# Performance work log

Measured on AMD Instinct MI355X. Metric: run time of the kernel, lower is better.

The kernel has to match this reference:

```python
import jax, jax.numpy as jnp
import numpy as np

N_NODES = 50000
N_EDGES = 800000
N_GRAPHS = 64
IN_DIM = 128
HID4 = 256  # hidden_dim * 4
OUT_DIM = 256
EPS = 1e-5


def setup_inputs() -> dict:
    key = jax.random.key(0)
    ks = jax.random.split(key, 11)
    x = jax.random.normal(ks[0], (N_NODES, IN_DIM), jnp.float32)
    w = jax.random.uniform(ks[1], (N_EDGES,), jnp.float32)
    src = jax.random.randint(ks[2], (N_EDGES,), 0, N_NODES, dtype=jnp.int32)
    dst = jax.random.randint(ks[3], (N_EDGES,), 0, N_NODES, dtype=jnp.int32)
    graph_ids = jnp.sort(jax.random.randint(ks[4], (N_NODES,), 0, N_GRAPHS, dtype=jnp.int32))
    W1 = jax.random.normal(ks[5], (IN_DIM, HID4), jnp.float32) * 0.05
    Wfc = jax.random.normal(ks[6], (IN_DIM, HID4), jnp.float32) * 0.05
    gamma = jnp.ones((HID4,), jnp.float32)
    beta = jnp.zeros((HID4,), jnp.float32)
    W2 = jax.random.normal(ks[7], (2 * HID4, HID4), jnp.float32) * 0.05
    W3 = jax.random.normal(ks[8], (HID4, OUT_DIM), jnp.float32) * 0.05
    return {"x": x, "w": w, "W1": W1, "Wfc": Wfc, "gamma": gamma, "beta": beta,
            "W2": W2, "W3": W3, "src": src, "dst": dst, "graph_ids": graph_ids}


def _agg(h, src, dst, w, n):
    # edge-weighted SpMM: sum_{e: dst(e)=v} w_e * h[src(e)]
    return jax.ops.segment_sum(h[src] * w[:, None], dst, num_segments=n)


def _graph_conv(h, W, src, dst, w, out_norm, in_norm, n):
    # DGL GraphConv, norm='both', no bias, with edge_weight.
    h = h * out_norm  # D_out^{-1/2} on source side
    din, dout = W.shape
    if din > dout:  # DGL applies W first when it shrinks the width
        h = _agg(h @ W, src, dst, w, n)
    else:
        h = _agg(h, src, dst, w, n) @ W
    return h * in_norm  # D_in^{-1/2} on destination side


def _layer_norm(h, gamma, beta):
    mu = jnp.mean(h, axis=-1, keepdims=True)
    var = jnp.var(h, axis=-1, keepdims=True)
    return (h - mu) * jax.lax.rsqrt(var + EPS) * gamma + beta


def reference(x, w, W1, Wfc, gamma, beta, W2, W3, src, dst, graph_ids):
    n = x.shape[0]
    ones_e = jnp.ones(src.shape[0], jnp.float32)
    out_deg = jnp.maximum(jax.ops.segment_sum(ones_e, src, num_segments=n), 1.0)
    in_deg = jnp.maximum(jax.ops.segment_sum(ones_e, dst, num_segments=n), 1.0)
    out_norm = (out_deg ** -0.5)[:, None]
    in_norm = (in_deg ** -0.5)[:, None]

    x1 = jax.nn.relu(_graph_conv(x, W1, src, dst, w, out_norm, in_norm, n))
    f1 = jax.nn.relu(_layer_norm(x @ Wfc, gamma, beta))
    x1f1 = jnp.concatenate((x1, f1), axis=1)  # [N, 512]
    x2 = jax.nn.relu(_graph_conv(x1f1, W2, src, dst, w, out_norm, in_norm, n))
    x3 = jax.nn.relu(_graph_conv(x2, W3, src, dst, w, out_norm, in_norm, n))
    # dgl.sum_nodes: per-graph segment-sum readout
    readout = jax.ops.segment_sum(x3, graph_ids, num_segments=N_GRAPHS)
    return readout
```

## Files before the change

kernel.cpp:

```cpp
#include <hip/hip_runtime.h>

#define NN 50000
#define NE 800000
#define NG 64
#define EPSF 1e-5f

typedef __bf16 bf16x8 __attribute__((ext_vector_type(8)));
typedef float f32x4 __attribute__((ext_vector_type(4)));

#define AS1 __attribute__((address_space(1)))
#define AS3 __attribute__((address_space(3)))

__device__ __forceinline__ void gl_lds16(const unsigned short* g, unsigned short* l) {
#if __has_builtin(__builtin_amdgcn_global_load_lds)
  __builtin_amdgcn_global_load_lds((const AS1 void*)g, (AS3 void*)l, 16, 0, 0);
#else
  *(uint4*)l = *(const uint4*)g;
#endif
}

__device__ __forceinline__ unsigned short f2bf(float f) {
  unsigned u = __builtin_bit_cast(unsigned, f);
  u += 0x7fff + ((u >> 16) & 1);
  return (unsigned short)(u >> 16);
}
__device__ __forceinline__ float bf_lo(unsigned u) {
  return __builtin_bit_cast(float, u << 16);
}
__device__ __forceinline__ float bf_hi(unsigned u) {
  return __builtin_bit_cast(float, u & 0xffff0000u);
}

#define NB_H 64
#define EC   12500
#define HWORDS 12500
#define XB   1563
#define XTOT 1600000
#define WTB  256
__global__ __launch_bounds__(1024) void prep_kernel(
    const int* __restrict__ src, const int* __restrict__ dst,
    unsigned char* __restrict__ hout, unsigned char* __restrict__ hin,
    int* __restrict__ rank,
    const float* __restrict__ x, unsigned short* __restrict__ xb,
    const float* __restrict__ W1, const float* __restrict__ Wfc,
    const float* __restrict__ W2, const float* __restrict__ W3,
    unsigned short* __restrict__ W1t, unsigned short* __restrict__ Wfct,
    unsigned short* __restrict__ W2t, unsigned short* __restrict__ W3t) {
  __shared__ unsigned hist[HWORDS];
  int b = blockIdx.x;
  int tid = threadIdx.x;
  if (b < NB_H) {
    int e0 = b * EC;
#pragma unroll
    for (int ph = 0; ph < 2; ph++) {
      const int* key = ph ? src : dst;
      unsigned char* gh = (ph ? hout : hin) + (size_t)b * NN;
      for (int i = tid; i < HWORDS; i += 1024) hist[i] = 0u;
      __syncthreads();
      for (int i = tid; i < EC; i += 1024) {
        int k = key[e0 + i];
        int sh = (k & 3) << 3;
        unsigned old = atomicAdd(&hist[k >> 2], 1u << sh);
        if (ph == 0) rank[e0 + i] = (int)((old >> sh) & 0xffu);
      }
      __syncthreads();
      unsigned* gw = (unsigned*)gh;
      for (int i = tid; i < HWORDS; i += 1024) gw[i] = hist[i];
      __syncthreads();
    }
  } else if (b < NB_H + XB) {
    int i = (b - NB_H) * 1024 + tid;
    if (i < XTOT) {
      float4 v = ((const float4*)x)[i];
      uint2 pk;
      pk.x = (unsigned)f2bf(v.x) | ((unsigned)f2bf(v.y) << 16);
      pk.y = (unsigned)f2bf(v.z) | ((unsigned)f2bf(v.w) << 16);
      ((uint2*)xb)[i] = pk;
    }
  } else {
    int i = (b - NB_H - XB) * 1024 + tid;
    const float* W; unsigned short* Wt; int K, local;
    if (i < 32768)       { W = W1;  Wt = W1t;  K = 128; local = i; }
    else if (i < 65536)  { W = Wfc; Wt = Wfct; K = 128; local = i - 32768; }
    else if (i < 196608) { W = W2;  Wt = W2t;  K = 512; local = i - 65536; }
    else                 { W = W3;  Wt = W3t;  K = 256; local = i - 196608; }
    int n = local / K, k = local - n * K;
    Wt[local] = f2bf(W[(size_t)k * 256 + n]);
  }
}

__global__ void norms_scan1(const unsigned char* __restrict__ hout,
                            unsigned char* __restrict__ hin,
                            int* __restrict__ din,
                            float* __restrict__ onorm, float* __restrict__ inorm,
                            int* __restrict__ bsum, int n) {
  int i = blockIdx.x * 256 + threadIdx.x;
  int d = 0;
  if (i < n) {
    int a = 0;
    for (int b = 0; b < NB_H; b++) a += hout[(size_t)b * NN + i];
    int run = 0;
    for (int b = 0; b < NB_H; b++) {
      int t = hin[(size_t)b * NN + i];
      hin[(size_t)b * NN + i] = (unsigned char)run;
      run += t;
    }
    d = run;
    din[i] = run;
    onorm[i] = rsqrtf((float)(a > 1 ? a : 1));
    inorm[i] = rsqrtf((float)(d > 1 ? d : 1));
  }
  int v = d;
#pragma unroll
  for (int off = 32; off > 0; off >>= 1) v += __shfl_down(v, off);
  __shared__ int ws[4];
  int wave = threadIdx.x >> 6, lane = threadIdx.x & 63;
  if (lane == 0) ws[wave] = v;
  __syncthreads();
  if (threadIdx.x == 0) bsum[blockIdx.x] = ws[0] + ws[1] + ws[2] + ws[3];
}

__global__ void scan3_kernel(const int* __restrict__ din, const int* __restrict__ bsum,
                             int* __restrict__ rp, int n, int nb) {
  int t = threadIdx.x;
  int lane = t & 63, wave = t >> 6;
  int bj = (t < nb) ? bsum[t] : 0;
  int pre = (t < (int)blockIdx.x) ? bj : 0;
  int p = pre, q = bj;
#pragma unroll
  for (int off = 32; off > 0; off >>= 1) {
    p += __shfl_down(p, off);
    q += __shfl_down(q, off);
  }
  __shared__ int red[8];
  __shared__ int baseS, totS;
  if (lane == 0) { red[wave] = p; red[4 + wave] = q; }
  __syncthreads();
  if (t == 0) {
    baseS = red[0] + red[1] + red[2] + red[3];
    totS  = red[4] + red[5] + red[6] + red[7];
  }
  __syncthreads();
  int i = blockIdx.x * 256 + t;
  int v = (i < n) ? din[i] : 0;
  __shared__ int tmp[256];
  tmp[t] = v;
  __syncthreads();
  for (int off = 1; off < 256; off <<= 1) {
    int x = (t >= off) ? tmp[t - off] : 0;
    __syncthreads();
    tmp[t] += x;
    __syncthreads();
  }
  if (i < n) rp[i] = tmp[t] - v + baseS;
  if (blockIdx.x == gridDim.x - 1 && t == 0) rp[n] = totS;
}

__global__ void fill_kernel(const int* __restrict__ src, const int* __restrict__ dst,
                            const float* __restrict__ w, const float* __restrict__ onorm,
                            const float* __restrict__ inorm,
                            const int* __restrict__ rp, const int* __restrict__ rank,
                            const unsigned char* __restrict__ binBase,
                            uint2* __restrict__ edge, int E) {
  int e = blockIdx.x * 256 + threadIdx.x;
  if (e < E) {
    int d = dst[e], s = src[e];
    int b = e / EC;
    int pos = rp[d] + (int)binBase[(size_t)b * NN + d] + rank[e];
    float wv = w[e] * onorm[s] * inorm[d];
    edge[pos] = make_uint2((unsigned)s, __builtin_bit_cast(unsigned, wv));
  }
}

template <int RELU, int NU>
__global__ __launch_bounds__(64) void spmm_bf16(
    const unsigned short* __restrict__ feat, int ldf,
    const int* __restrict__ rp, const uint2* __restrict__ edge,
    unsigned short* __restrict__ out, int ldo) {
  int v = blockIdx.x;
  int t = threadIdx.x;
  int beg = rp[v], end = rp[v + 1];
  float acc[2 * NU];
#pragma unroll
  for (int i = 0; i < 2 * NU; i++) acc[i] = 0.f;
  const unsigned short* base = feat + t * (2 * NU);
  int e = beg;
  for (; e + 8 <= end; e += 8) {
    int s[8]; float ww[8];
#pragma unroll
    for (int k = 0; k < 8; k++) {
      uint2 q = edge[e + k];
      s[k] = (int)q.x;
      ww[k] = __builtin_bit_cast(float, q.y);
    }
    unsigned u[8][NU];
#pragma unroll
    for (int k = 0; k < 8; k++) {
      const unsigned* pr = (const unsigned*)&base[(size_t)s[k] * ldf];
      if (NU == 2) { uint2 q = *(const uint2*)pr; u[k][0] = q.x; u[k][NU - 1] = q.y; }
      else u[k][0] = pr[0];
    }
#pragma unroll
    for (int k = 0; k < 8; k++)
#pragma unroll
      for (int j = 0; j < NU; j++) {
        acc[2 * j]     += ww[k] * bf_lo(u[k][j]);
        acc[2 * j + 1] += ww[k] * bf_hi(u[k][j]);
      }
  }
  for (; e < end; e++) {
    uint2 qe = edge[e];
    float w0 = __builtin_bit_cast(float, qe.y);
    const unsigned* pr = (const unsigned*)&base[(size_t)qe.x * ldf];
    unsigned u[NU];
    if (NU == 2) { uint2 q = *(const uint2*)pr; u[0] = q.x; u[NU - 1] = q.y; }
    else u[0] = pr[0];
#pragma unroll
    for (int j = 0; j < NU; j++) {
      acc[2 * j]     += w0 * bf_lo(u[j]);
      acc[2 * j + 1] += w0 * bf_hi(u[j]);
    }
  }
  unsigned o[NU];
#pragma unroll
  for (int j = 0; j < NU; j++) {
    float a = acc[2 * j], b = acc[2 * j + 1];
    if (RELU) { a = fmaxf(a, 0.f); b = fmaxf(b, 0.f); }
    o[j] = (unsigned)f2bf(a) | ((unsigned)f2bf(b) << 16);
  }
  unsigned* po = (unsigned*)&out[(size_t)v * ldo + t * (2 * NU)];
  if (NU == 2) *(uint2*)po = make_uint2(o[0], o[NU - 1]);
  else po[0] = o[0];
}

__device__ __forceinline__ void gemm_db_body(
    const unsigned short* __restrict__ A, int lda,
    const unsigned short* __restrict__ Bt, int K,
    unsigned short* __restrict__ C, int ldc, int col_off, int M,
    int relu, unsigned short (*As)[8192], unsigned short (*Bs)[8192]) {
  const int tid = threadIdx.x;
  const int lane = tid & 63;
  const int w = tid >> 6;
  const int wm = w >> 1, wn = w & 1;
  const int m0 = blockIdx.x * 128;
  const int n0 = blockIdx.y * 128;
  const int q = lane >> 4;
  const int r16 = lane & 15;

  f32x4 acc[4][4];
#pragma unroll
  for (int i = 0; i < 4; i++)
#pragma unroll
    for (int j = 0; j < 4; j++) acc[i][j] = (f32x4){0.f, 0.f, 0.f, 0.f};

  const unsigned short* pa[4];
  const unsigned short* pb[4];
#pragma unroll
  for (int i = 0; i < 4; i++) {
    int ch = i * 256 + tid;
    int sub = ch >> 6, sl = ch & 63;
    int mi = sub >> 1, kk = sub & 1;
    int row = mi * 16 + (sl & 15);
    int kc = kk * 32 + (sl >> 4) * 8;
    int gm = m0 + row; if (gm >= M) gm = M - 1;
    pa[i] = A + (size_t)gm * lda + kc;
    int gn = n0 + row;
    pb[i] = Bt + (size_t)gn * K + kc;
  }

  const int NT = K >> 6;
#pragma unroll
  for (int i = 0; i < 4; i++) {
    int ch8 = (i * 256 + tid) * 8;
    gl_lds16(pa[i], &As[0][ch8]);
    gl_lds16(pb[i], &Bs[0][ch8]);
  }
  __syncthreads();

  int cur = 0;
  for (int t = 0; t < NT; t++) {
    if (t + 1 < NT) {
      int nk = (t + 1) << 6;
#pragma unroll
      for (int i = 0; i < 4; i++) {
        int ch8 = (i * 256 + tid) * 8;
        gl_lds16(pa[i] + nk, &As[cur ^ 1][ch8]);
        gl_lds16(pb[i] + nk, &Bs[cur ^ 1][ch8]);
      }
    }
#pragma unroll
    for (int kk = 0; kk < 2; kk++) {
      bf16x8 af[4], bfr[4];
#pragma unroll
      for (int i = 0; i < 4; i++)
        af[i] = *(const bf16x8*)&As[cur][((wm * 4 + i) * 2 + kk) * 512 + lane * 8];
#pragma unroll
      for (int j = 0; j < 4; j++)
        bfr[j] = *(const bf16x8*)&Bs[cur][((wn * 4 + j) * 2 + kk) * 512 + lane * 8];
#pragma unroll
      for (int i = 0; i < 4; i++)
#pragma unroll
        for (int j = 0; j < 4; j++)
          acc[i][j] = __builtin_amdgcn_mfma_f32_16x16x32_bf16(af[i], bfr[j], acc[i][j], 0, 0, 0);
    }
    __syncthreads();
    cur ^= 1;
  }

#pragma unroll
  for (int i = 0; i < 4; i++) {
    int rbase = m0 + wm * 64 + i * 16 + q * 4;
#pragma unroll
    for (int r = 0; r < 4; r++) {
      int gm = rbase + r;
      if (gm >= M) continue;
#pragma unroll
      for (int j = 0; j < 4; j++) {
        float v = acc[i][j][r];
        if (relu) v = fmaxf(v, 0.f);
        int gn = col_off + n0 + wn * 64 + j * 16 + r16;
        C[(size_t)gm * ldc + gn] = f2bf(v);
      }
    }
  }
}

__global__ __launch_bounds__(256) void gemm12_kernel(
    const unsigned short* __restrict__ A0, const unsigned short* __restrict__ B0,
    const unsigned short* __restrict__ A1, const unsigned short* __restrict__ B1,
    unsigned short* __restrict__ C, int M) {
  __shared__ unsigned short As[2][8192];
  __shared__ unsigned short Bs[2][8192];
  int z = blockIdx.z;
  gemm_db_body(z ? A1 : A0, 128, z ? B1 : B0, 128, C, 512, z * 256, M, z == 0, As, Bs);
}

__global__ __launch_bounds__(256) void gemm_kernel(
    const unsigned short* __restrict__ A, int lda,
    const unsigned short* __restrict__ Bt, int K,
    unsigned short* __restrict__ C, int ldc, int M, int relu) {
  __shared__ unsigned short As[2][8192];
  __shared__ unsigned short Bs[2][8192];
  gemm_db_body(A, lda, Bt, K, C, ldc, 0, M, relu, As, Bs);
}

__global__ void ln_relu_bf16(unsigned short* __restrict__ h, int ld,
                             const float* __restrict__ gamma,
                             const float* __restrict__ beta) {
  int v = blockIdx.x;
  int f = threadIdx.x;
  float val = bf_lo((unsigned)h[(size_t)v * ld + f]);
  float s = val, qq = val * val;
#pragma unroll
  for (int off = 32; off > 0; off >>= 1) {
    s += __shfl_down(s, off);
    qq += __shfl_down(qq, off);
  }
  __shared__ float ws_[5], wq_[5];
  int wave = f >> 6, lane = f & 63;
  if (lane == 0) { ws_[wave] = s; wq_[wave] = qq; }
  __syncthreads();
  if (f == 0) {
    float S = 0, Q = 0;
    for (int i = 0; i < 4; i++) { S += ws_[i]; Q += wq_[i]; }
    ws_[4] = S; wq_[4] = Q;
  }
  __syncthreads();
  float mean = ws_[4] * (1.f / 256.f);
  float var = wq_[4] * (1.f / 256.f) - mean * mean;
  float y = (val - mean) * rsqrtf(var + EPSF) * gamma[f] + beta[f];
  h[(size_t)v * ld + f] = f2bf(y > 0.f ? y : 0.f);
}

__global__ void readout_kernel(const unsigned short* __restrict__ x3,
                               const int* __restrict__ gid,
                               float* __restrict__ out, int n) {
  int g = blockIdx.x;
  int part = blockIdx.y;
  int f = threadIdx.x;
  int lo = 0, hi = n;
  while (lo < hi) { int mid = (lo + hi) >> 1; if (gid[mid] < g) lo = mid + 1; else hi = mid; }
  int s = lo;
  lo = s; hi = n;
  while (lo < hi) { int mid = (lo + hi) >> 1; if (gid[mid] < g + 1) lo = mid + 1; else hi = mid; }
  int e = lo;
  int len = e - s;
  if (len <= 0) return;
  int chunk = (len + 7) / 8;
  int cs = s + part * chunk;
  int ce = cs + chunk; if (ce > e) ce = e;
  if (cs >= ce) return;
  float acc = 0.f;
  for (int v = cs; v < ce; v++) acc += bf_lo((unsigned)x3[(size_t)v * 256 + f]);
  atomicAdd(&out[g * 256 + f], acc);
}


extern "C" void kernel_launch(void* const* d_in, const int* in_sizes, int n_in,
                              void* d_out, int out_size, void* d_ws, size_t ws_size,
                              hipStream_t stream) {
  const float* x     = (const float*)d_in[0];
  const float* w     = (const float*)d_in[1];
  const float* W1    = (const float*)d_in[2];
  const float* Wfc   = (const float*)d_in[3];
  const float* gamma = (const float*)d_in[4];
  const float* beta  = (const float*)d_in[5];
  const float* W2    = (const float*)d_in[6];
  const float* W3    = (const float*)d_in[7];
  const int*   src   = (const int*)d_in[8];
  const int*   dst   = (const int*)d_in[9];
  const int*   gid   = (const int*)d_in[10];
  float* out = (float*)d_out;

  const int N = NN, E = NE;

  char* p = (char*)d_ws;
  auto alloc = [&](size_t bytes) {
    char* r = p;
    p += (bytes + 255) & ~(size_t)255;
    return r;
  };
  unsigned char* hout = (unsigned char*)alloc((size_t)NB_H * N);
  unsigned char* hin  = (unsigned char*)alloc((size_t)NB_H * N);
  int*   din     = (int*)alloc((size_t)N * 4);
  float* onorm   = (float*)alloc((size_t)N * 4);
  float* inorm   = (float*)alloc((size_t)N * 4);
  int*   row_ptr = (int*)alloc((size_t)(N + 1) * 4);
  int*   bsum    = (int*)alloc(256 * 4);
  int*   rank    = (int*)alloc((size_t)E * 4);
  uint2* edge    = (uint2*)alloc((size_t)E * 8);
  unsigned short* xb    = (unsigned short*)alloc((size_t)N * 128 * 2);
  unsigned short* aggX  = (unsigned short*)alloc((size_t)N * 128 * 2);
  unsigned short* x1f1  = (unsigned short*)alloc((size_t)N * 512 * 2);
  unsigned short* y2    = (unsigned short*)alloc((size_t)N * 256 * 2);
  unsigned short* x2    = (unsigned short*)alloc((size_t)N * 256 * 2);
  unsigned short* aggx2 = (unsigned short*)alloc((size_t)N * 256 * 2);
  unsigned short* W1t   = (unsigned short*)alloc((size_t)256 * 128 * 2);
  unsigned short* Wfct  = (unsigned short*)alloc((size_t)256 * 128 * 2);
  unsigned short* W2t   = (unsigned short*)alloc((size_t)256 * 512 * 2);
  unsigned short* W3t   = (unsigned short*)alloc((size_t)256 * 256 * 2);
  unsigned short* x3 = x1f1;

  hipMemsetAsync(out, 0, (size_t)NG * 256 * 4, stream);

  const int nbS = (N + 255) / 256;

  prep_kernel<<<NB_H + XB + WTB, 1024, 0, stream>>>(src, dst, hout, hin, rank,
                                                    x, xb, W1, Wfc, W2, W3,
                                                    W1t, Wfct, W2t, W3t);
  norms_scan1<<<nbS, 256, 0, stream>>>(hout, hin, din, onorm, inorm, bsum, N);
  scan3_kernel<<<nbS, 256, 0, stream>>>(din, bsum, row_ptr, N, nbS);
  fill_kernel<<<(E + 255) / 256, 256, 0, stream>>>(src, dst, w, onorm, inorm, row_ptr,
                                                   rank, hin, edge, E);

  dim3 ggrid((N + 127) / 128, 2);
  dim3 ggridz((N + 127) / 128, 2, 2);

  spmm_bf16<0, 1><<<N, 64, 0, stream>>>(xb, 128, row_ptr, edge, aggX, 128);
  gemm12_kernel<<<ggridz, 256, 0, stream>>>(aggX, W1t, xb, Wfct, x1f1, N);
  ln_relu_bf16<<<N, 256, 0, stream>>>(x1f1 + 256, 512, gamma, beta);
  gemm_kernel<<<ggrid, 256, 0, stream>>>(x1f1, 512, W2t, 512, y2, 256, N, 0);
  spmm_bf16<1, 2><<<N, 64, 0, stream>>>(y2, 256, row_ptr, edge, x2, 256);
  spmm_bf16<0, 2><<<N, 64, 0, stream>>>(x2, 256, row_ptr, edge, aggx2, 256);
  gemm_kernel<<<ggrid, 256, 0, stream>>>(aggx2, 256, W3t, 256, x3, 256, N, 1);
  readout_kernel<<<dim3(NG, 8), 256, 0, stream>>>(x3, gid, out, N);
}
```

Measured before the change: 432.8 us.

## Fuse LayerNorm into FC GEMM and graph readout into final GEMM epilogue

New measurement: 404.1 us. 1.07x faster.

```diff
diff --git a/kernel.cpp b/kernel.cpp
--- a/kernel.cpp
+++ b/kernel.cpp
@@ -233,21 +233,17 @@
   else po[0] = o[0];
 }
 
-__device__ __forceinline__ void gemm_db_body(
+__device__ __forceinline__ void gemm_core(
     const unsigned short* __restrict__ A, int lda,
-    const unsigned short* __restrict__ Bt, int K,
-    unsigned short* __restrict__ C, int ldc, int col_off, int M,
-    int relu, unsigned short (*As)[8192], unsigned short (*Bs)[8192]) {
+    const unsigned short* __restrict__ Bt, int K, int M,
+    int bm, int bn, int relu,
+    unsigned short (*As)[8192], unsigned short (*Bs)[8192],
+    f32x4 (&acc)[4][4]) {
   const int tid = threadIdx.x;
   const int lane = tid & 63;
-  const int w = tid >> 6;
-  const int wm = w >> 1, wn = w & 1;
-  const int m0 = blockIdx.x * 128;
-  const int n0 = blockIdx.y * 128;
-  const int q = lane >> 4;
-  const int r16 = lane & 15;
-
-  f32x4 acc[4][4];
+  const int m0 = bm * 128;
+  const int n0 = bn * 128;
+
 #pragma unroll
   for (int i = 0; i < 4; i++)
 #pragma unroll
@@ -277,6 +273,8 @@
   }
   __syncthreads();
 
+  const int wv = tid >> 6;
+  const int wm = wv >> 1, wn = wv & 1;
   int cur = 0;
   for (int t = 0; t < NT; t++) {
     if (t + 1 < NT) {
@@ -306,7 +304,25 @@
     __syncthreads();
     cur ^= 1;
   }
-
+  if (relu) {
+#pragma unroll
+    for (int i = 0; i < 4; i++)
+#pragma unroll
+      for (int j = 0; j < 4; j++)
+#pragma unroll
+        for (int r = 0; r < 4; r++) acc[i][j][r] = fmaxf(acc[i][j][r], 0.f);
+  }
+}
+
+__device__ __forceinline__ void gemm_store(
+    const f32x4 (&acc)[4][4], unsigned short* __restrict__ C, int ldc,
+    int col_off, int M, int bm, int bn) {
+  const int tid = threadIdx.x;
+  const int lane = tid & 63;
+  const int wv = tid >> 6;
+  const int wm = wv >> 1, wn = wv & 1;
+  const int q = lane >> 4, r16 = lane & 15;
+  const int m0 = bm * 128, n0 = bn * 128;
 #pragma unroll
   for (int i = 0; i < 4; i++) {
     int rbase = m0 + wm * 64 + i * 16 + q * 4;
@@ -316,23 +332,142 @@
       if (gm >= M) continue;
 #pragma unroll
       for (int j = 0; j < 4; j++) {
-        float v = acc[i][j][r];
-        if (relu) v = fmaxf(v, 0.f);
         int gn = col_off + n0 + wn * 64 + j * 16 + r16;
-        C[(size_t)gm * ldc + gn] = f2bf(v);
-      }
-    }
-  }
-}
-
-__global__ __launch_bounds__(256) void gemm12_kernel(
+        C[(size_t)gm * ldc + gn] = f2bf(acc[i][j][r]);
+      }
+    }
+  }
+}
+
+__device__ __forceinline__ void fcln_body(
+    const unsigned short* __restrict__ A, const unsigned short* __restrict__ Bt,
+    const float* __restrict__ gamma, const float* __restrict__ beta,
+    unsigned short* __restrict__ C, int M, unsigned short* lds) {
+  const int tid = threadIdx.x;
+  const int lane = tid & 63;
+  const int w = tid >> 6;
+  const int q = lane >> 4, r16 = lane & 15;
+  const int m0 = blockIdx.x * 64;
+  unsigned short* As = lds;
+  unsigned short* Bs = lds + 8192;
+
+#pragma unroll
+  for (int i = 0; i < 4; i++) {
+    int ch = i * 256 + tid;
+    int st = ch >> 6, sl = ch & 63;
+    int mi = st >> 2, kk = st & 3;
+    int gm = m0 + mi * 16 + (sl & 15); if (gm >= M) gm = M - 1;
+    int k = kk * 32 + (sl >> 4) * 8;
+    gl_lds16(A + (size_t)gm * 128 + k, &As[ch * 8]);
+  }
+#pragma unroll
+  for (int i = 0; i < 16; i++) {
+    int ch = i * 256 + tid;
+    int st = ch >> 6, sl = ch & 63;
+    int ns = st >> 2, kk = st & 3;
+    int n = ns * 16 + (sl & 15);
+    int k = kk * 32 + (sl >> 4) * 8;
+    gl_lds16(Bt + (size_t)n * 128 + k, &Bs[ch * 8]);
+  }
+  __syncthreads();
+
+  f32x4 acc[4][4];
+#pragma unroll
+  for (int i = 0; i < 4; i++)
+#pragma unroll
+    for (int j = 0; j < 4; j++) acc[i][j] = (f32x4){0.f, 0.f, 0.f, 0.f};
+
+#pragma unroll
+  for (int kk = 0; kk < 4; kk++) {
+    bf16x8 af[4], bfr[4];
+#pragma unroll
+    for (int i = 0; i < 4; i++)
+      af[i] = *(const bf16x8*)&As[(i * 4 + kk) * 512 + lane * 8];
+#pragma unroll
+    for (int j = 0; j < 4; j++)
+      bfr[j] = *(const bf16x8*)&Bs[((w * 4 + j) * 4 + kk) * 512 + lane * 8];
+#pragma unroll
+    for (int i = 0; i < 4; i++)
+#pragma unroll
+      for (int j = 0; j < 4; j++)
+        acc[i][j] = __builtin_amdgcn_mfma_f32_16x16x32_bf16(af[i], bfr[j], acc[i][j], 0, 0, 0);
+  }
+  __syncthreads();
+
+  float* fws = (float*)lds;
+  float* fwq = fws + 256;
+  float* fmean = fwq + 256;
+  float* frs = fmean + 64;
+
+#pragma unroll
+  for (int i = 0; i < 4; i++)
+#pragma unroll
+    for (int r = 0; r < 4; r++) {
+      float s  = acc[i][0][r] + acc[i][1][r] + acc[i][2][r] + acc[i][3][r];
+      float q2 = acc[i][0][r] * acc[i][0][r] + acc[i][1][r] * acc[i][1][r] +
+                 acc[i][2][r] * acc[i][2][r] + acc[i][3][r] * acc[i][3][r];
+#pragma unroll
+      for (int off = 8; off > 0; off >>= 1) {
+        s  += __shfl_down(s, off, 16);
+        q2 += __shfl_down(q2, off, 16);
+      }
+      if (r16 == 0) {
+        int row = i * 16 + q * 4 + r;
+        fws[w * 64 + row] = s;
+        fwq[w * 64 + row] = q2;
+      }
+    }
+  __syncthreads();
+  if (tid < 64) {
+    float S = fws[tid] + fws[64 + tid] + fws[128 + tid] + fws[192 + tid];
+    float Q = fwq[tid] + fwq[64 + tid] + fwq[128 + tid] + fwq[192 + tid];
+    float mean = S * (1.f / 256.f);
+    float var = Q * (1.f / 256.f) - mean * mean;
+    fmean[tid] = mean;
+    frs[tid] = rsqrtf(var + EPSF);
+  }
+  __syncthreads();
+
+  float g4[4], b4[4];
+#pragma unroll
+  for (int j = 0; j < 4; j++) {
+    int c = w * 64 + j * 16 + r16;
+    g4[j] = gamma[c];
+    b4[j] = beta[c];
+  }
+#pragma unroll
+  for (int i = 0; i < 4; i++)
+#pragma unroll
+    for (int r = 0; r < 4; r++) {
+      int row = i * 16 + q * 4 + r;
+      int gm = m0 + row;
+      if (gm >= M) continue;
+      float mean = fmean[row], rs = frs[row];
+#pragma unroll
+      for (int j = 0; j < 4; j++) {
+        int c = w * 64 + j * 16 + r16;
+        float y = (acc[i][j][r] - mean) * rs * g4[j] + b4[j];
+        C[(size_t)gm * 512 + 256 + c] = f2bf(fmaxf(y, 0.f));
+      }
+    }
+}
+
+__global__ __launch_bounds__(256) void g12f_kernel(
     const unsigned short* __restrict__ A0, const unsigned short* __restrict__ B0,
     const unsigned short* __restrict__ A1, const unsigned short* __restrict__ B1,
+    const float* __restrict__ gamma, const float* __restrict__ beta,
     unsigned short* __restrict__ C, int M) {
-  __shared__ unsigned short As[2][8192];
-  __shared__ unsigned short Bs[2][8192];
-  int z = blockIdx.z;
-  gemm_db_body(z ? A1 : A0, 128, z ? B1 : B0, 128, C, 512, z * 256, M, z == 0, As, Bs);
+  __shared__ unsigned short lds[40960];
+  if (blockIdx.z == 0) {
+    f32x4 acc[4][4];
+    int bm = blockIdx.x >> 1, bn = blockIdx.x & 1;
+    gemm_core(A0, 128, B0, 128, M, bm, bn, 1,
+              (unsigned short (*)[8192])lds,
+              (unsigned short (*)[8192])(lds + 16384), acc);
+    gemm_store(acc, C, 512, 0, M, bm, bn);
+  } else {
+    fcln_body(A1, B1, gamma, beta, C, M, lds);
+  }
 }
 
 __global__ __launch_bounds__(256) void gemm_kernel(
@@ -341,58 +476,65 @@
     unsigned short* __restrict__ C, int ldc, int M, int relu) {
   __shared__ unsigned short As[2][8192];
   __shared__ unsigned short Bs[2][8192];
-  gemm_db_body(A, lda, Bt, K, C, ldc, 0, M, relu, As, Bs);
-}
-
-__global__ void ln_relu_bf16(unsigned short* __restrict__ h, int ld,
-                             const float* __restrict__ gamma,
-                             const float* __restrict__ beta) {
-  int v = blockIdx.x;
-  int f = threadIdx.x;
-  float val = bf_lo((unsigned)h[(size_t)v * ld + f]);
-  float s = val, qq = val * val;
-#pragma unroll
-  for (int off = 32; off > 0; off >>= 1) {
-    s += __shfl_down(s, off);
-    qq += __shfl_down(qq, off);
-  }
-  __shared__ float ws_[5], wq_[5];
-  int wave = f >> 6, lane = f & 63;
-  if (lane == 0) { ws_[wave] = s; wq_[wave] = qq; }
-  __syncthreads();
-  if (f == 0) {
-    float S = 0, Q = 0;
-    for (int i = 0; i < 4; i++) { S += ws_[i]; Q += wq_[i]; }
-    ws_[4] = S; wq_[4] = Q;
-  }
-  __syncthreads();
-  float mean = ws_[4] * (1.f / 256.f);
-  float var = wq_[4] * (1.f / 256.f) - mean * mean;
-  float y = (val - mean) * rsqrtf(var + EPSF) * gamma[f] + beta[f];
-  h[(size_t)v * ld + f] = f2bf(y > 0.f ? y : 0.f);
-}
-
-__global__ void readout_kernel(const unsigned short* __restrict__ x3,
-                               const int* __restrict__ gid,
-                               float* __restrict__ out, int n) {
-  int g = blockIdx.x;
-  int part = blockIdx.y;
-  int f = threadIdx.x;
-  int lo = 0, hi = n;
-  while (lo < hi) { int mid = (lo + hi) >> 1; if (gid[mid] < g) lo = mid + 1; else hi = mid; }
-  int s = lo;
-  lo = s; hi = n;
-  while (lo < hi) { int mid = (lo + hi) >> 1; if (gid[mid] < g + 1) lo = mid + 1; else hi = mid; }
-  int e = lo;
-  int len = e - s;
-  if (len <= 0) return;
-  int chunk = (len + 7) / 8;
-  int cs = s + part * chunk;
-  int ce = cs + chunk; if (ce > e) ce = e;
-  if (cs >= ce) return;
-  float acc = 0.f;
-  for (int v = cs; v < ce; v++) acc += bf_lo((unsigned)x3[(size_t)v * 256 + f]);
-  atomicAdd(&out[g * 256 + f], acc);
+  f32x4 acc[4][4];
+  gemm_core(A, lda, Bt, K, M, blockIdx.x, blockIdx.y, relu, As, Bs, acc);
+  gemm_store(acc, C, ldc, 0, M, blockIdx.x, blockIdx.y);
+}
+
+__global__ __launch_bounds__(256) void gemm_ro_kernel(
+    const unsigned short* __restrict__ A,
+    const unsigned short* __restrict__ Bt,
+    const int* __restrict__ gid, float* __restrict__ out, int M) {
+  __shared__ unsigned short As[2][8192];
+  __shared__ unsigned short Bs[2][8192];
+  __shared__ float red[8][128];
+  f32x4 acc[4][4];
+  gemm_core(A, 256, Bt, 256, M, blockIdx.x, blockIdx.y, 1, As, Bs, acc);
+
+  const int tid = threadIdx.x;
+  const int lane = tid & 63;
+  const int wv = tid >> 6;
+  const int wm = wv >> 1, wn = wv & 1;
+  const int q = lane >> 4, r16 = lane & 15;
+  const int m0 = blockIdx.x * 128, n0 = blockIdx.y * 128;
+
+  int gids[4][4];
+#pragma unroll
+  for (int i = 0; i < 4; i++)
+#pragma unroll
+    for (int r = 0; r < 4; r++) {
+      int gm = m0 + wm * 64 + i * 16 + q * 4 + r;
+      gids[i][r] = (gm < M) ? gid[gm] : -1;
+    }
+  int lastrow = m0 + 127; if (lastrow >= M) lastrow = M - 1;
+  int g0 = gid[m0];
+  int g1 = gid[lastrow];
+
+  for (int base = g0; base <= g1; base += 8) {
+    for (int idx = tid; idx < 1024; idx += 256) ((float*)red)[idx] = 0.f;
+    __syncthreads();
+#pragma unroll
+    for (int i = 0; i < 4; i++)
+#pragma unroll
+      for (int r = 0; r < 4; r++) {
+        int g = gids[i][r] - base;
+        if ((unsigned)g < 8u) {
+#pragma unroll
+          for (int j = 0; j < 4; j++) {
+            float v = acc[i][j][r];
+            if (v != 0.f) atomicAdd(&red[g][wn * 64 + j * 16 + r16], v);
+          }
+        }
+      }
+    __syncthreads();
+    int nf = g1 - base + 1; if (nf > 8) nf = 8;
+    for (int idx = tid; idx < nf * 128; idx += 256) {
+      int g = idx >> 7, c = idx & 127;
+      float v = red[g][c];
+      if (v != 0.f) atomicAdd(&out[(base + g) * 256 + n0 + c], v);
+    }
+    __syncthreads();
+  }
 }
 
 
@@ -439,7 +581,6 @@
   unsigned short* Wfct  = (unsigned short*)alloc((size_t)256 * 128 * 2);
   unsigned short* W2t   = (unsigned short*)alloc((size_t)256 * 512 * 2);
   unsigned short* W3t   = (unsigned short*)alloc((size_t)256 * 256 * 2);
-  unsigned short* x3 = x1f1;
 
   hipMemsetAsync(out, 0, (size_t)NG * 256 * 4, stream);
 
@@ -454,14 +595,11 @@
                                                    rank, hin, edge, E);
 
   dim3 ggrid((N + 127) / 128, 2);
-  dim3 ggridz((N + 127) / 128, 2, 2);
 
   spmm_bf16<0, 1><<<N, 64, 0, stream>>>(xb, 128, row_ptr, edge, aggX, 128);
-  gemm12_kernel<<<ggridz, 256, 0, stream>>>(aggX, W1t, xb, Wfct, x1f1, N);
-  ln_relu_bf16<<<N, 256, 0, stream>>>(x1f1 + 256, 512, gamma, beta);
+  g12f_kernel<<<dim3(782, 1, 2), 256, 0, stream>>>(aggX, W1t, xb, Wfct, gamma, beta, x1f1, N);
   gemm_kernel<<<ggrid, 256, 0, stream>>>(x1f1, 512, W2t, 512, y2, 256, N, 0);
   spmm_bf16<1, 2><<<N, 64, 0, stream>>>(y2, 256, row_ptr, edge, x2, 256);
   spmm_bf16<0, 2><<<N, 64, 0, stream>>>(x2, 256, row_ptr, edge, aggx2, 256);
-  gemm_kernel<<<ggrid, 256, 0, stream>>>(aggx2, 256, W3t, 256, x3, 256, N, 1);
-  readout_kernel<<<dim3(NG, 8), 256, 0, stream>>>(x3, gid, out, N);
-}
+  gemm_ro_kernel<<<ggrid, 256, 0, stream>>>(aggx2, W3t, gid, out, N);
+}
```

## Fuse final GEMM with per-graph readout and halve GEMM K-tile

Applied to the files above, without the earlier changes.

Result: slower. 446.3 us (+3.1%).

```diff
diff --git a/kernel.cpp b/kernel.cpp
--- a/kernel.cpp
+++ b/kernel.cpp
@@ -233,80 +233,92 @@
   else po[0] = o[0];
 }
 
-__device__ __forceinline__ void gemm_db_body(
+__device__ __forceinline__ void gemm_core32(
     const unsigned short* __restrict__ A, int lda,
-    const unsigned short* __restrict__ Bt, int K,
-    unsigned short* __restrict__ C, int ldc, int col_off, int M,
-    int relu, unsigned short (*As)[8192], unsigned short (*Bs)[8192]) {
+    const unsigned short* __restrict__ Bt, int K, int M,
+    int bm, int bn, int relu,
+    unsigned short (*As)[4096], unsigned short (*Bs)[4096],
+    f32x4 (&acc)[4][4]) {
   const int tid = threadIdx.x;
   const int lane = tid & 63;
-  const int w = tid >> 6;
-  const int wm = w >> 1, wn = w & 1;
-  const int m0 = blockIdx.x * 128;
-  const int n0 = blockIdx.y * 128;
-  const int q = lane >> 4;
-  const int r16 = lane & 15;
-
-  f32x4 acc[4][4];
+  const int m0 = bm * 128;
+  const int n0 = bn * 128;
+
 #pragma unroll
   for (int i = 0; i < 4; i++)
 #pragma unroll
     for (int j = 0; j < 4; j++) acc[i][j] = (f32x4){0.f, 0.f, 0.f, 0.f};
 
-  const unsigned short* pa[4];
-  const unsigned short* pb[4];
-#pragma unroll
-  for (int i = 0; i < 4; i++) {
+  const unsigned short* pa[2];
+  const unsigned short* pb[2];
+#pragma unroll
+  for (int i = 0; i < 2; i++) {
     int ch = i * 256 + tid;
     int sub = ch >> 6, sl = ch & 63;
-    int mi = sub >> 1, kk = sub & 1;
-    int row = mi * 16 + (sl & 15);
-    int kc = kk * 32 + (sl >> 4) * 8;
+    int row = sub * 16 + (sl & 15);
+    int kc = (sl >> 4) * 8;
     int gm = m0 + row; if (gm >= M) gm = M - 1;
     pa[i] = A + (size_t)gm * lda + kc;
     int gn = n0 + row;
     pb[i] = Bt + (size_t)gn * K + kc;
   }
 
-  const int NT = K >> 6;
-#pragma unroll
-  for (int i = 0; i < 4; i++) {
+  const int NT = K >> 5;
+#pragma unroll
+  for (int i = 0; i < 2; i++) {
     int ch8 = (i * 256 + tid) * 8;
     gl_lds16(pa[i], &As[0][ch8]);
     gl_lds16(pb[i], &Bs[0][ch8]);
   }
   __syncthreads();
 
+  const int wv = tid >> 6;
+  const int wm = wv >> 1, wn = wv & 1;
   int cur = 0;
   for (int t = 0; t < NT; t++) {
     if (t + 1 < NT) {
-      int nk = (t + 1) << 6;
-#pragma unroll
-      for (int i = 0; i < 4; i++) {
+      int nk = (t + 1) << 5;
+#pragma unroll
+      for (int i = 0; i < 2; i++) {
         int ch8 = (i * 256 + tid) * 8;
         gl_lds16(pa[i] + nk, &As[cur ^ 1][ch8]);
         gl_lds16(pb[i] + nk, &Bs[cur ^ 1][ch8]);
       }
     }
-#pragma unroll
-    for (int kk = 0; kk < 2; kk++) {
-      bf16x8 af[4], bfr[4];
-#pragma unroll
-      for (int i = 0; i < 4; i++)
-        af[i] = *(const bf16x8*)&As[cur][((wm * 4 + i) * 2 + kk) * 512 + lane * 8];
+    bf16x8 af[4], bfr[4];
+#pragma unroll
+    for (int i = 0; i < 4; i++)
+      af[i] = *(const bf16x8*)&As[cur][(wm * 4 + i) * 512 + lane * 8];
+#pragma unroll
+    for (int j = 0; j < 4; j++)
+      bfr[j] = *(const bf16x8*)&Bs[cur][(wn * 4 + j) * 512 + lane * 8];
+#pragma unroll
+    for (int i = 0; i < 4; i++)
 #pragma unroll
       for (int j = 0; j < 4; j++)
-        bfr[j] = *(const bf16x8*)&Bs[cur][((wn * 4 + j) * 2 + kk) * 512 + lane * 8];
-#pragma unroll
-      for (int i = 0; i < 4; i++)
-#pragma unroll
-        for (int j = 0; j < 4; j++)
-          acc[i][j] = __builtin_amdgcn_mfma_f32_16x16x32_bf16(af[i], bfr[j], acc[i][j], 0, 0, 0);
-    }
+        acc[i][j] = __builtin_amdgcn_mfma_f32_16x16x32_bf16(af[i], bfr[j], acc[i][j], 0, 0, 0);
     __syncthreads();
     cur ^= 1;
   }
-
+  if (relu) {
+#pragma unroll
+    for (int i = 0; i < 4; i++)
+#pragma unroll
+      for (int j = 0; j < 4; j++)
+#pragma unroll
+        for (int r = 0; r < 4; r++) acc[i][j][r] = fmaxf(acc[i][j][r], 0.f);
+  }
+}
+
+__device__ __forceinline__ void gemm_store(
+    const f32x4 (&acc)[4][4], unsigned short* __restrict__ C, int ldc,
+    int col_off, int M, int bm, int bn) {
+  const int tid = threadIdx.x;
+  const int lane = tid & 63;
+  const int wv = tid >> 6;
+  const int wm = wv >> 1, wn = wv & 1;
+  const int q = lane >> 4, r16 = lane & 15;
+  const int m0 = bm * 128, n0 = bn * 128;
 #pragma unroll
   for (int i = 0; i < 4; i++) {
     int rbase = m0 + wm * 64 + i * 16 + q * 4;
@@ -316,32 +328,91 @@
       if (gm >= M) continue;
 #pragma unroll
       for (int j = 0; j < 4; j++) {
-        float v = acc[i][j][r];
-        if (relu) v = fmaxf(v, 0.f);
         int gn = col_off + n0 + wn * 64 + j * 16 + r16;
-        C[(size_t)gm * ldc + gn] = f2bf(v);
+        C[(size_t)gm * ldc + gn] = f2bf(acc[i][j][r]);
       }
     }
   }
 }
 
-__global__ __launch_bounds__(256) void gemm12_kernel(
+__global__ __launch_bounds__(256) void g12_kernel(
     const unsigned short* __restrict__ A0, const unsigned short* __restrict__ B0,
     const unsigned short* __restrict__ A1, const unsigned short* __restrict__ B1,
     unsigned short* __restrict__ C, int M) {
-  __shared__ unsigned short As[2][8192];
-  __shared__ unsigned short Bs[2][8192];
+  __shared__ unsigned short As[2][4096];
+  __shared__ unsigned short Bs[2][4096];
+  f32x4 acc[4][4];
   int z = blockIdx.z;
-  gemm_db_body(z ? A1 : A0, 128, z ? B1 : B0, 128, C, 512, z * 256, M, z == 0, As, Bs);
+  gemm_core32(z ? A1 : A0, 128, z ? B1 : B0, 128, M,
+              blockIdx.x, blockIdx.y, z == 0, As, Bs, acc);
+  gemm_store(acc, C, 512, z * 256, M, blockIdx.x, blockIdx.y);
 }
 
 __global__ __launch_bounds__(256) void gemm_kernel(
     const unsigned short* __restrict__ A, int lda,
     const unsigned short* __restrict__ Bt, int K,
     unsigned short* __restrict__ C, int ldc, int M, int relu) {
-  __shared__ unsigned short As[2][8192];
-  __shared__ unsigned short Bs[2][8192];
-  gemm_db_body(A, lda, Bt, K, C, ldc, 0, M, relu, As, Bs);
+  __shared__ unsigned short As[2][4096];
+  __shared__ unsigned short Bs[2][4096];
+  f32x4 acc[4][4];
+  gemm_core32(A, lda, Bt, K, M, blockIdx.x, blockIdx.y, relu, As, Bs, acc);
+  gemm_store(acc, C, ldc, 0, M, blockIdx.x, blockIdx.y);
+}
+
+__global__ __launch_bounds__(256) void gemm_ro_kernel(
+    const unsigned short* __restrict__ A,
+    const unsigned short* __restrict__ Bt,
+    const int* __restrict__ gid, float* __restrict__ out, int M) {
+  __shared__ unsigned short As[2][4096];
+  __shared__ unsigned short Bs[2][4096];
+  __shared__ float red[8][128];
+  f32x4 acc[4][4];
+  gemm_core32(A, 256, Bt, 256, M, blockIdx.x, blockIdx.y, 1, As, Bs, acc);
+
+  const int tid = threadIdx.x;
+  const int lane = tid & 63;
+  const int wv = tid >> 6;
+  const int wm = wv >> 1, wn = wv & 1;
+  const int q = lane >> 4, r16 = lane & 15;
+  const int m0 = blockIdx.x * 128, n0 = blockIdx.y * 128;
+
+  int gids[4][4];
+#pragma unroll
+  for (int i = 0; i < 4; i++)
+#pragma unroll
+    for (int r = 0; r < 4; r++) {
+      int gm = m0 + wm * 64 + i * 16 + q * 4 + r;
+      gids[i][r] = (gm < M) ? gid[gm] : -1;
+    }
+  int lastrow = m0 + 127; if (lastrow >= M) lastrow = M - 1;
+  int g0 = gid[m0];
+  int g1 = gid[lastrow];
+
+  for (int base = g0; base <= g1; base += 8) {
+    for (int idx = tid; idx < 1024; idx += 256) ((float*)red)[idx] = 0.f;
+    __syncthreads();
+#pragma unroll
+    for (int i = 0; i < 4; i++)
+#pragma unroll
+      for (int r = 0; r < 4; r++) {
+        int g = gids[i][r] - base;
+        if ((unsigned)g < 8u) {
+#pragma unroll
+          for (int j = 0; j < 4; j++) {
+            float v = acc[i][j][r];
+            if (v != 0.f) atomicAdd(&red[g][wn * 64 + j * 16 + r16], v);
+          }
+        }
+      }
+    __syncthreads();
+    int nf = g1 - base + 1; if (nf > 8) nf = 8;
+    for (int idx = tid; idx < nf * 128; idx += 256) {
+      int g = idx >> 7, c = idx & 127;
+      float v = red[g][c];
+      if (v != 0.f) atomicAdd(&out[(base + g) * 256 + n0 + c], v);
+    }
+    __syncthreads();
+  }
 }
 
 __global__ void ln_relu_bf16(unsigned short* __restrict__ h, int ld,
@@ -370,29 +441,6 @@
   float var = wq_[4] * (1.f / 256.f) - mean * mean;
   float y = (val - mean) * rsqrtf(var + EPSF) * gamma[f] + beta[f];
   h[(size_t)v * ld + f] = f2bf(y > 0.f ? y : 0.f);
-}
-
-__global__ void readout_kernel(const unsigned short* __restrict__ x3,
-                               const int* __restrict__ gid,
-                               float* __restrict__ out, int n) {
-  int g = blockIdx.x;
-  int part = blockIdx.y;
-  int f = threadIdx.x;
-  int lo = 0, hi = n;
-  while (lo < hi) { int mid = (lo + hi) >> 1; if (gid[mid] < g) lo = mid + 1; else hi = mid; }
-  int s = lo;
-  lo = s; hi = n;
-  while (lo < hi) { int mid = (lo + hi) >> 1; if (gid[mid] < g + 1) lo = mid + 1; else hi = mid; }
-  int e = lo;
-  int len = e - s;
-  if (len <= 0) return;
-  int chunk = (len + 7) / 8;
-  int cs = s + part * chunk;
-  int ce = cs + chunk; if (ce > e) ce = e;
-  if (cs >= ce) return;
-  float acc = 0.f;
-  for (int v = cs; v < ce; v++) acc += bf_lo((unsigned)x3[(size_t)v * 256 + f]);
-  atomicAdd(&out[g * 256 + f], acc);
 }
 
 
@@ -439,7 +487,6 @@
   unsigned short* Wfct  = (unsigned short*)alloc((size_t)256 * 128 * 2);
   unsigned short* W2t   = (unsigned short*)alloc((size_t)256 * 512 * 2);
   unsigned short* W3t   = (unsigned short*)alloc((size_t)256 * 256 * 2);
-  unsigned short* x3 = x1f1;
 
   hipMemsetAsync(out, 0, (size_t)NG * 256 * 4, stream);
 
@@ -457,11 +504,10 @@
   dim3 ggridz((N + 127) / 128, 2, 2);
 
   spmm_bf16<0, 1><<<N, 64, 0, stream>>>(xb, 128, row_ptr, edge, aggX, 128);
-  gemm12_kernel<<<ggridz, 256, 0, stream>>>(aggX, W1t, xb, Wfct, x1f1, N);
+  g12_kernel<<<ggridz, 256, 0, stream>>>(aggX, W1t, xb, Wfct, x1f1, N);
   ln_relu_bf16<<<N, 256, 0, stream>>>(x1f1 + 256, 512, gamma, beta);
   gemm_kernel<<<ggrid, 256, 0, stream>>>(x1f1, 512, W2t, 512, y2, 256, N, 0);
   spmm_bf16<1, 2><<<N, 64, 0, stream>>>(y2, 256, row_ptr, edge, x2, 256);
   spmm_bf16<0, 2><<<N, 64, 0, stream>>>(x2, 256, row_ptr, edge, aggx2, 256);
-  gemm_kernel<<<ggrid, 256, 0, stream>>>(aggx2, 256, W3t, 256, x3, 256, N, 1);
-  readout_kernel<<<dim3(NG, 8), 256, 0, stream>>>(x3, gid, out, N);
-}
+  gemm_ro_kernel<<<ggrid, 256, 0, stream>>>(aggx2, W3t, gid, out, N);
+}
```
